# Optimization experiments

Measured on AMD Instinct MI355X. Metric: run time of the kernel, lower is better.

## Reference

```python
import jax, jax.numpy as jnp
import numpy as np

NUM_HEADS = 4
HEAD_DIM = 64  # base_dim(256) // num_heads(4)
NEG_INF = -1e9  # stand-in for float('-inf') masked_fill; avoids NaN if a row is fully masked


def setup_inputs() -> dict:
    key = jax.random.key(0)
    ks = jax.random.split(key, 12)
    B, S, T, D, U = 512, 128, 24, 256, 100000
    return {
        "timeslot_embedded": jax.random.normal(ks[0], (T, D), jnp.float32),
        "user": jax.random.randint(ks[1], (B,), 0, U),
        "hour": jax.random.randint(ks[2], (B, S), 0, T),
        "hour_mask": jax.random.randint(ks[3], (B, S, T), 0, 2).astype(jnp.int32),
        "user_pref_table": jax.random.normal(ks[4], (U, D), jnp.float32),
        "Wq": jax.random.normal(ks[5], (2 * D, D), jnp.float32) * 0.05,
        "bq": jax.random.normal(ks[6], (D,), jnp.float32) * 0.05,
        "Wk": jax.random.normal(ks[7], (D, D), jnp.float32) * 0.05,
        "bk": jax.random.normal(ks[8], (D,), jnp.float32) * 0.05,
        "Wv": jax.random.normal(ks[9], (D, D), jnp.float32) * 0.05,
        "bv": jax.random.normal(ks[10], (D,), jnp.float32) * 0.05,
        "Wu": jax.random.normal(ks[11], (D, D), jnp.float32) * 0.05,
        "bu": jnp.zeros((D,), jnp.float32),
    }


def reference(timeslot_embedded, user, hour, hour_mask, user_pref_table,
              Wq, bq, Wk, bk, Wv, bv, Wu, bu):
    B, S = hour.shape
    T, D = timeslot_embedded.shape
    N = B * S
    hour_flat = hour.reshape(N)                       # [N]
    mask = hour_mask.reshape(N, T)                    # [N, T]

    # user preference broadcast over sequence, then flatten: [N, D]
    user_feat = jnp.broadcast_to(user_pref_table[user][:, None, :], (B, S, D)).reshape(N, D)
    time_feat = timeslot_embedded[hour_flat]          # [N, D]
    query = jnp.concatenate([user_feat, time_feat], axis=-1)  # [N, 2D]

    # all heads at once (stacked per-head linears)
    q = (query @ Wq + bq).reshape(N, NUM_HEADS, HEAD_DIM)             # [N, H, hd]
    k = (timeslot_embedded @ Wk + bk).reshape(T, NUM_HEADS, HEAD_DIM)  # [T, H, hd]
    v = (timeslot_embedded @ Wv + bv).reshape(T, NUM_HEADS, HEAD_DIM)  # [T, H, hd]

    scale = 1.0 / np.sqrt(HEAD_DIM).astype(np.float32)
    scores = jnp.einsum('nhd,thd->nht', q, k) * scale                 # [N, H, T]
    scores = jnp.where(mask[:, None, :] == 1, NEG_INF, scores)
    attn = jax.nn.softmax(scores, axis=-1)
    heads = jnp.einsum('nht,thd->nhd', attn, v).reshape(N, D)         # concat heads
    out = heads @ Wu + bu                                             # unify_heads
    return out.reshape(B, S, D)
```

## Files before the change

### kernel.cpp

```cpp
#include <hip/hip_runtime.h>
#include <math.h>

#define B_   512
#define S_   128
#define T_   24
#define D_   256
#define H_   4
#define HD_  64
#define N_   (B_*S_)
#define NEG_INF_ -1e9f

typedef unsigned int  u32;
typedef unsigned short u16;
typedef _Float16 f16;
typedef _Float16 f16x8 __attribute__((ext_vector_type(8)));
typedef float    f32x4 __attribute__((ext_vector_type(4)));
typedef u32      u32x4 __attribute__((ext_vector_type(4)));

#define OFF_K    0
#define OFF_V    6144
#define OFF_QT   12288
#define OFF_ST   18432
#define OFF_SU   20736
#define OFF_VUT  69888

__device__ inline u32 pack2f16(float a, float b) {
    u16 ha = __builtin_bit_cast(u16, (f16)a);
    u16 hb = __builtin_bit_cast(u16, (f16)b);
    return (u32)ha | ((u32)hb << 16);
}

__global__ void precompute1(const float* __restrict__ ts,
                            const float* __restrict__ Wk, const float* __restrict__ bk,
                            const float* __restrict__ Wv, const float* __restrict__ bv,
                            const float* __restrict__ Wq, const float* __restrict__ bq,
                            float* __restrict__ ws) {
    int blk = blockIdx.x;
    int mat = blk / T_;
    int t   = blk % T_;
    int d   = threadIdx.x;
    const float* W; const float* bias; float* dst;
    if (mat == 0)      { W = Wk;           bias = bk; dst = ws + OFF_K;  }
    else if (mat == 1) { W = Wv;           bias = bv; dst = ws + OFF_V;  }
    else               { W = Wq + D_*D_;   bias = bq; dst = ws + OFF_QT; }
    float acc = bias[d];
    #pragma unroll 8
    for (int j = 0; j < D_; ++j)
        acc += ts[t*D_ + j] * W[j*D_ + d];
    dst[t*D_ + d] = acc;
}

__global__ void precompute2(const float* __restrict__ Wu, float* __restrict__ ws) {
    const float* v  = ws + OFF_V;
    const float* k  = ws + OFF_K;
    const float* qt = ws + OFF_QT;
    int blk = blockIdx.x;
    if (blk < 96) {
        int h = blk / T_, t = blk % T_;
        int d = threadIdx.x;
        float acc = 0.f;
        #pragma unroll 8
        for (int l = 0; l < HD_; ++l)
            acc += v[t*D_ + h*HD_ + l] * Wu[(h*HD_ + l)*D_ + d];
        u16* vuT = (u16*)(ws + OFF_VUT);
        vuT[d*96 + h*T_ + t] = __builtin_bit_cast(u16, (f16)acc);
    } else {
        for (int i = 0; i < 9; ++i) {
            int idx = threadIdx.x*9 + i;
            int tp = idx / 96; int rem = idx % 96;
            int h = rem / T_, t = rem % T_;
            float acc = 0.f;
            #pragma unroll 8
            for (int l = 0; l < HD_; ++l)
                acc += qt[tp*D_ + h*HD_ + l] * k[t*D_ + h*HD_ + l];
            ws[OFF_ST + idx] = acc;
        }
    }
}

__global__ void user_su(const int* __restrict__ user,
                        const float* __restrict__ upref,
                        const float* __restrict__ Wq,
                        float* __restrict__ ws) {
    __shared__ float qu[D_];
    int b = blockIdx.x;
    int d = threadIdx.x;
    int u = user[b];
    const float* up = upref + (size_t)u * D_;
    float acc = 0.f;
    #pragma unroll 8
    for (int j = 0; j < D_; ++j)
        acc += up[j] * Wq[j*D_ + d];
    qu[d] = acc;
    __syncthreads();
    if (d < 96) {
        int h = d / T_, t = d % T_;
        const float* k = ws + OFF_K;
        float s = 0.f;
        #pragma unroll 8
        for (int l = 0; l < HD_; ++l)
            s += qu[h*HD_ + l] * k[t*D_ + h*HD_ + l];
        ws[OFF_SU + b*96 + d] = s;
    }
}

__global__ __launch_bounds__(256) void fused_attn_out(
        const int* __restrict__ hour,
        const int* __restrict__ hmask,
        const float* __restrict__ ws,
        const float* __restrict__ bu,
        float* __restrict__ out) {
    __shared__ __align__(16) u32 atile[3072];
    int tid = threadIdx.x;
    int n0  = blockIdx.x * 64;
    int b   = n0 >> 7;

    {
        int r = tid >> 2, h = tid & 3;
        int n = n0 + r;
        int hr = hour[n];
        const float4* su4 = (const float4*)(ws + OFF_SU + b*96  + h*T_);
        const float4* st4 = (const float4*)(ws + OFF_ST + hr*96 + h*T_);
        const int4*   m4  = (const int4*)(hmask + (size_t)n * T_);
        float s[T_];
        float mx = -3.0e38f;
        #pragma unroll
        for (int i = 0; i < 6; ++i) {
            float4 a = su4[i];
            float4 c = st4[i];
            int4   m = m4[i];
            float v0 = (m.x == 1) ? NEG_INF_ : (a.x + c.x) * 0.125f;
            float v1 = (m.y == 1) ? NEG_INF_ : (a.y + c.y) * 0.125f;
            float v2 = (m.z == 1) ? NEG_INF_ : (a.z + c.z) * 0.125f;
            float v3 = (m.w == 1) ? NEG_INF_ : (a.w + c.w) * 0.125f;
            s[4*i+0] = v0; s[4*i+1] = v1; s[4*i+2] = v2; s[4*i+3] = v3;
            mx = fmaxf(mx, fmaxf(fmaxf(v0, v1), fmaxf(v2, v3)));
        }
        float sum = 0.f;
        #pragma unroll
        for (int t = 0; t < T_; ++t) {
            float e = __expf(s[t] - mx);
            s[t] = e; sum += e;
        }
        float inv = 1.f / sum;
        int mtile = r >> 4, rlane = r & 15;
        #pragma unroll
        for (int i = 0; i < 12; ++i) {
            int t = 2*i;
            int k = 24*h + t;
            int ktile = k >> 5;
            int kg    = (k >> 3) & 3;
            int j2    = (k & 7) >> 1;
            atile[((mtile*3 + ktile)*64 + kg*16 + rlane)*4 + j2] =
                pack2f16(s[t]*inv, s[t+1]*inv);
        }
    }
    __syncthreads();

    {
        int w  = tid >> 6;
        int l  = tid & 63;
        int lhi = l >> 4, llo = l & 15;
        const u16* vuT = (const u16*)(ws + OFF_VUT);

        f16x8 bf[4][3];
        #pragma unroll
        for (int nt = 0; nt < 4; ++nt) {
            int col = w*64 + nt*16 + llo;
            #pragma unroll
            for (int kt = 0; kt < 3; ++kt) {
                u32x4 bv = *(const u32x4*)(vuT + col*96 + kt*32 + lhi*8);
                bf[nt][kt] = __builtin_bit_cast(f16x8, bv);
            }
        }

        f32x4 acc[4][4];
        #pragma unroll
        for (int mt = 0; mt < 4; ++mt)
            #pragma unroll
            for (int nt = 0; nt < 4; ++nt)
                acc[mt][nt] = (f32x4){0.f, 0.f, 0.f, 0.f};

        #pragma unroll
        for (int mt = 0; mt < 4; ++mt) {
            f16x8 af[3];
            #pragma unroll
            for (int kt = 0; kt < 3; ++kt) {
                u32x4 av = *(const u32x4*)&atile[((mt*3 + kt)*64 + l)*4];
                af[kt] = __builtin_bit_cast(f16x8, av);
            }
            #pragma unroll
            for (int nt = 0; nt < 4; ++nt) {
                f32x4 c = acc[mt][nt];
                c = __builtin_amdgcn_mfma_f32_16x16x32_f16(af[0], bf[nt][0], c, 0, 0, 0);
                c = __builtin_amdgcn_mfma_f32_16x16x32_f16(af[1], bf[nt][1], c, 0, 0, 0);
                c = __builtin_amdgcn_mfma_f32_16x16x32_f16(af[2], bf[nt][2], c, 0, 0, 0);
                acc[mt][nt] = c;
            }
        }

        float bias[4];
        #pragma unroll
        for (int nt = 0; nt < 4; ++nt) bias[nt] = bu[w*64 + nt*16 + llo];
        float* op = out + (size_t)n0 * D_ + w*64 + llo;
        #pragma unroll
        for (int mt = 0; mt < 4; ++mt)
            #pragma unroll
            for (int nt = 0; nt < 4; ++nt)
                #pragma unroll
                for (int q = 0; q < 4; ++q)
                    op[(size_t)(mt*16 + lhi*4 + q) * D_ + nt*16] = acc[mt][nt][q] + bias[nt];
    }
}

extern "C" void kernel_launch(void* const* d_in, const int* in_sizes, int n_in,
                              void* d_out, int out_size, void* d_ws, size_t ws_size,
                              hipStream_t stream) {
    const float* ts    = (const float*)d_in[0];
    const int*   user  = (const int*)  d_in[1];
    const int*   hour  = (const int*)  d_in[2];
    const int*   hmask = (const int*)  d_in[3];
    const float* upref = (const float*)d_in[4];
    const float* Wq    = (const float*)d_in[5];
    const float* bq    = (const float*)d_in[6];
    const float* Wk    = (const float*)d_in[7];
    const float* bk    = (const float*)d_in[8];
    const float* Wv    = (const float*)d_in[9];
    const float* bv    = (const float*)d_in[10];
    const float* Wu    = (const float*)d_in[11];
    const float* bu    = (const float*)d_in[12];
    float* out = (float*)d_out;
    float* ws  = (float*)d_ws;

    precompute1<<<72, 256, 0, stream>>>(ts, Wk, bk, Wv, bv, Wq, bq, ws);
    precompute2<<<97, 256, 0, stream>>>(Wu, ws);
    user_su<<<B_, 256, 0, stream>>>(user, upref, Wq, ws);
    fused_attn_out<<<N_/64, 256, 0, stream>>>(hour, hmask, ws, bu, out);
}
```

Before: 245.4 us.

## Merge precompute kernels into two stages and use nontemporal output stores

Folds the per-user query projection into the first precompute kernel and the per-user score computation into the second, so the precompute runs as two launches instead of three and the user work runs in parallel with the timeslot work. The user query vectors now go through a new workspace region instead of shared memory. Unroll factors rise and the main kernel's output writes become nontemporal stores to avoid cache pollution. The cost is extra workspace traffic for the intermediate user query vectors.

```diff
diff --git a/kernel.cpp b/kernel.cpp
--- a/kernel.cpp
+++ b/kernel.cpp
@@ -20,9 +20,10 @@
 #define OFF_K    0
 #define OFF_V    6144
 #define OFF_QT   12288
-#define OFF_ST   18432
-#define OFF_SU   20736
-#define OFF_VUT  69888
+#define OFF_QU   18432
+#define OFF_ST   149504
+#define OFF_SU   151808
+#define OFF_VUT  200960
 
 __device__ inline u32 pack2f16(float a, float b) {
     u16 ha = __builtin_bit_cast(u16, (f16)a);
@@ -30,27 +31,42 @@
     return (u32)ha | ((u32)hb << 16);
 }
 
-__global__ void precompute1(const float* __restrict__ ts,
-                            const float* __restrict__ Wk, const float* __restrict__ bk,
-                            const float* __restrict__ Wv, const float* __restrict__ bv,
-                            const float* __restrict__ Wq, const float* __restrict__ bq,
-                            float* __restrict__ ws) {
+__global__ __launch_bounds__(256) void stage1(
+        const float* __restrict__ ts,
+        const int*   __restrict__ user,
+        const float* __restrict__ upref,
+        const float* __restrict__ Wk, const float* __restrict__ bk,
+        const float* __restrict__ Wv, const float* __restrict__ bv,
+        const float* __restrict__ Wq, const float* __restrict__ bq,
+        float* __restrict__ ws) {
     int blk = blockIdx.x;
-    int mat = blk / T_;
-    int t   = blk % T_;
     int d   = threadIdx.x;
-    const float* W; const float* bias; float* dst;
-    if (mat == 0)      { W = Wk;           bias = bk; dst = ws + OFF_K;  }
-    else if (mat == 1) { W = Wv;           bias = bv; dst = ws + OFF_V;  }
-    else               { W = Wq + D_*D_;   bias = bq; dst = ws + OFF_QT; }
-    float acc = bias[d];
-    #pragma unroll 8
+    const float* src; const float* W; float acc; float* dst;
+    if (blk < 72) {
+        int mat = blk / T_;
+        int t   = blk % T_;
+        const float* bias;
+        if (mat == 0)      { W = Wk;         bias = bk; dst = ws + OFF_K  + t*D_; }
+        else if (mat == 1) { W = Wv;         bias = bv; dst = ws + OFF_V  + t*D_; }
+        else               { W = Wq + D_*D_; bias = bq; dst = ws + OFF_QT + t*D_; }
+        src = ts + t*D_;
+        acc = bias[d];
+    } else {
+        int b = blk - 72;
+        int u = user[b];
+        src = upref + (size_t)u * D_;
+        W   = Wq;
+        dst = ws + OFF_QU + b*D_;
+        acc = 0.f;
+    }
+    #pragma unroll 16
     for (int j = 0; j < D_; ++j)
-        acc += ts[t*D_ + j] * W[j*D_ + d];
-    dst[t*D_ + d] = acc;
-}
-
-__global__ void precompute2(const float* __restrict__ Wu, float* __restrict__ ws) {
+        acc += src[j] * W[j*D_ + d];
+    dst[d] = acc;
+}
+
+__global__ __launch_bounds__(256) void stage2(
+        const float* __restrict__ Wu, float* __restrict__ ws) {
     const float* v  = ws + OFF_V;
     const float* k  = ws + OFF_K;
     const float* qt = ws + OFF_QT;
@@ -59,48 +75,34 @@
         int h = blk / T_, t = blk % T_;
         int d = threadIdx.x;
         float acc = 0.f;
-        #pragma unroll 8
+        #pragma unroll 16
         for (int l = 0; l < HD_; ++l)
             acc += v[t*D_ + h*HD_ + l] * Wu[(h*HD_ + l)*D_ + d];
         u16* vuT = (u16*)(ws + OFF_VUT);
         vuT[d*96 + h*T_ + t] = __builtin_bit_cast(u16, (f16)acc);
-    } else {
+    } else if (blk == 96) {
         for (int i = 0; i < 9; ++i) {
             int idx = threadIdx.x*9 + i;
             int tp = idx / 96; int rem = idx % 96;
             int h = rem / T_, t = rem % T_;
             float acc = 0.f;
-            #pragma unroll 8
+            #pragma unroll 16
             for (int l = 0; l < HD_; ++l)
                 acc += qt[tp*D_ + h*HD_ + l] * k[t*D_ + h*HD_ + l];
             ws[OFF_ST + idx] = acc;
         }
-    }
-}
-
-__global__ void user_su(const int* __restrict__ user,
-                        const float* __restrict__ upref,
-                        const float* __restrict__ Wq,
-                        float* __restrict__ ws) {
-    __shared__ float qu[D_];
-    int b = blockIdx.x;
-    int d = threadIdx.x;
-    int u = user[b];
-    const float* up = upref + (size_t)u * D_;
-    float acc = 0.f;
-    #pragma unroll 8
-    for (int j = 0; j < D_; ++j)
-        acc += up[j] * Wq[j*D_ + d];
-    qu[d] = acc;
-    __syncthreads();
-    if (d < 96) {
-        int h = d / T_, t = d % T_;
-        const float* k = ws + OFF_K;
-        float s = 0.f;
-        #pragma unroll 8
-        for (int l = 0; l < HD_; ++l)
-            s += qu[h*HD_ + l] * k[t*D_ + h*HD_ + l];
-        ws[OFF_SU + b*96 + d] = s;
+    } else {
+        int b = blk - 97;
+        int d = threadIdx.x;
+        if (d < 96) {
+            int h = d / T_, t = d % T_;
+            const float* qu = ws + OFF_QU + b*D_;
+            float s = 0.f;
+            #pragma unroll 16
+            for (int l = 0; l < HD_; ++l)
+                s += qu[h*HD_ + l] * k[t*D_ + h*HD_ + l];
+            ws[OFF_SU + b*96 + d] = s;
+        }
     }
 }
 
@@ -209,7 +211,8 @@
             for (int nt = 0; nt < 4; ++nt)
                 #pragma unroll
                 for (int q = 0; q < 4; ++q)
-                    op[(size_t)(mt*16 + lhi*4 + q) * D_ + nt*16] = acc[mt][nt][q] + bias[nt];
+                    __builtin_nontemporal_store(acc[mt][nt][q] + bias[nt],
+                        &op[(size_t)(mt*16 + lhi*4 + q) * D_ + nt*16]);
     }
 }
 
@@ -232,8 +235,7 @@
     float* out = (float*)d_out;
     float* ws  = (float*)d_ws;
 
-    precompute1<<<72, 256, 0, stream>>>(ts, Wk, bk, Wv, bv, Wq, bq, ws);
-    precompute2<<<97, 256, 0, stream>>>(Wu, ws);
-    user_su<<<B_, 256, 0, stream>>>(user, upref, Wq, ws);
+    stage1<<<584, 256, 0, stream>>>(ts, user, upref, Wk, bk, Wv, bv, Wq, bq, ws);
+    stage2<<<609, 256, 0, stream>>>(Wu, ws);
     fused_attn_out<<<N_/64, 256, 0, stream>>>(hour, hmask, ws, bu, out);
 }
```

Result: faster. 224.2 us (-8.7%).
